# Kernel optimization log

Hardware: AMD Instinct MI355X
Metric: run time of the kernel (lower is better)

Reference implementation:

```python
import jax, jax.numpy as jnp
import numpy as np

B, N, NPOINT, NSAMPLE = 8, 8192, 2048, 64
RADIUS = 0.2
C_IN = 64  # input feature channels; mlp[0]=64 -> 67 after use_xyz concat


def setup_inputs() -> dict:
    key = jax.random.key(0)
    ks = jax.random.split(key, 12)
    xyz = jax.random.uniform(ks[0], (B, N, 3), dtype=jnp.float32)
    features = jax.random.normal(ks[1], (B, N, C_IN), dtype=jnp.float32)
    inds = jax.random.randint(ks[2], (B, NPOINT), 0, N, dtype=jnp.int32)

    def mkw(k, cin, cout):
        return jax.random.normal(k, (cin, cout), jnp.float32) * (1.0 / np.sqrt(cin).astype(np.float32))

    w0 = mkw(ks[3], C_IN + 3, 64)
    w1 = mkw(ks[4], 64, 64)
    w2 = mkw(ks[5], 64, 128)
    # BN (inference) folded into per-channel scale/shift
    s0 = 1.0 + 0.1 * jax.random.normal(ks[6], (64,), jnp.float32)
    t0 = 0.1 * jax.random.normal(ks[7], (64,), jnp.float32)
    s1 = 1.0 + 0.1 * jax.random.normal(ks[8], (64,), jnp.float32)
    t1 = 0.1 * jax.random.normal(ks[9], (64,), jnp.float32)
    s2 = 1.0 + 0.1 * jax.random.normal(ks[10], (128,), jnp.float32)
    t2 = 0.1 * jax.random.normal(ks[11], (128,), jnp.float32)
    return dict(xyz=xyz, features=features, inds=inds,
                w0=w0, s0=s0, t0=t0, w1=w1, s1=s1, t1=t1, w2=w2, s2=s2, t2=t2)


def _ball_query(xyz, new_xyz):
    """First NSAMPLE point indices within RADIUS of each query; pad by repeating
    the first hit (matches CUDA ball_query semantics). xyz:(B,N,3) new_xyz:(B,S,3)."""
    nn = jnp.sum(xyz * xyz, axis=-1)            # (B,N)
    qq = jnp.sum(new_xyz * new_xyz, axis=-1)    # (B,S)
    d2 = qq[:, :, None] + nn[:, None, :] - 2.0 * jnp.einsum('bsc,bnc->bsn', new_xyz, xyz)
    within = d2 < (RADIUS * RADIUS)
    ar = jnp.arange(N, dtype=jnp.int32)
    keyed = jnp.where(within, ar[None, None, :], N)   # out-of-radius -> sentinel N
    keyed = jnp.sort(keyed, axis=-1)[:, :, :NSAMPLE]  # first hits in point order
    idx = jnp.where(keyed == N, keyed[:, :, :1], keyed)
    return jnp.minimum(idx, N - 1)


_gather = jax.vmap(lambda pts, i: pts[i])  # (N,C),(M,) -> (M,C) per batch


def reference(xyz, features, inds, w0, s0, t0, w1, s1, t1, w2, s2, t2):
    new_xyz = _gather(xyz, inds)                              # (B,S,3)
    idx = _ball_query(xyz, new_xyz)                           # (B,S,ns)
    flat = idx.reshape(B, NPOINT * NSAMPLE)
    g_xyz = _gather(xyz, flat).reshape(B, NPOINT, NSAMPLE, 3)
    g_xyz = (g_xyz - new_xyz[:, :, None, :]) / RADIUS         # normalize_xyz
    g_feat = _gather(features, flat).reshape(B, NPOINT, NSAMPLE, C_IN)
    x = jnp.concatenate([g_xyz, g_feat], axis=-1)             # (B,S,ns,C+3)
    for wgt, s, t in ((w0, s0, t0), (w1, s1, t1), (w2, s2, t2)):
        x = jax.nn.relu(jnp.einsum('bpsc,cd->bpsd', x, wgt) * s + t)
    new_features = jnp.max(x, axis=2)                         # max-pool over nsample
    return new_xyz, new_features, inds, idx
```

## Files before the change

kernel.cpp:

```cpp
#include <hip/hip_runtime.h>

#define BB 8
#define NN 8192
#define NPOINT 2048
#define NSAMPLE 64
#define CIN 64
#define RADIUS 0.2f
#define R2 (RADIUS * RADIUS)

#define OFF_NEWXYZ 0
#define OFF_FEAT (BB * NPOINT * 3)
#define OFF_INDS (OFF_FEAT + BB * NPOINT * 128)
#define OFF_IDX (OFF_INDS + BB * NPOINT)

typedef _Float16 half8 __attribute__((ext_vector_type(8)));
typedef _Float16 half4 __attribute__((ext_vector_type(4)));
typedef __fp16 f16x2 __attribute__((ext_vector_type(2)));
typedef float floatx16 __attribute__((ext_vector_type(16)));
typedef unsigned int uint2v __attribute__((ext_vector_type(2)));

#define P0 88
#define P1 72
#define X_LOC 0
#define H_LOC (64 * P0)
#define XH_WAVE (64 * P0 + 64 * P1)
#define WT0_S 0
#define WT1_S (64 * P0)
#define WT2_S (64 * P0 + 64 * P1)

#define QPW_FB 8
#define QPW_G 2

#define WSF16H (BB * NN * CIN)
#define WT0_OFF WSF16H
#define WT1_OFF (WT0_OFF + 64 * 80)
#define WT2_OFF (WT1_OFF + 64 * 64)
#define WS_END (WT2_OFF + 128 * 64)
#define WS_NEED ((size_t)WS_END * 2)

__global__ __launch_bounds__(256) void ballq_kernel(
    const float* __restrict__ xyz, const int* __restrict__ inds,
    float* __restrict__ out, const float* __restrict__ features,
    _Float16* __restrict__ ws16, const float* __restrict__ w0,
    const float* __restrict__ s0, const float* __restrict__ t0,
    const float* __restrict__ w1, const float* __restrict__ s1,
    const float* __restrict__ w2, const float* __restrict__ s2) {
  if (ws16) {
    const int t = blockIdx.x * 256 + threadIdx.x;
    const float4* src = (const float4*)features;
    const float4 a = src[2 * t + 0];
    const float4 b = src[2 * t + 1];
    union {
      half8 v;
      f16x2 p[4];
    } u;
    u.p[0] = __builtin_amdgcn_cvt_pkrtz(a.x, a.y);
    u.p[1] = __builtin_amdgcn_cvt_pkrtz(a.z, a.w);
    u.p[2] = __builtin_amdgcn_cvt_pkrtz(b.x, b.y);
    u.p[3] = __builtin_amdgcn_cvt_pkrtz(b.z, b.w);
    ((half8*)ws16)[t] = u.v;
    if (blockIdx.x == 0) {
      const int tt = threadIdx.x;
      if (tt < 64) {
        const int d = tt;
        const float sd = s0[d], td = t0[d];
        _Float16* row = ws16 + WT0_OFF + d * 80;
        for (int c = 0; c < 80; ++c) {
          float v = 0.0f;
          if (c < 64) v = w0[(3 + c) * 64 + d] * sd;
          else if (c < 67) v = w0[(c - 64) * 64 + d] * sd;
          else if (c == 67) v = td;
          row[c] = (_Float16)v;
        }
      } else if (tt < 128) {
        const int d = tt - 64;
        const float sd = s1[d];
        _Float16* row = ws16 + WT1_OFF + d * 64;
        for (int c = 0; c < 64; ++c) row[c] = (_Float16)(w1[c * 64 + d] * sd);
      } else {
        const int d2 = tt - 128;
        const float sd = s2[d2];
        _Float16* row = ws16 + WT2_OFF + d2 * 64;
        for (int c = 0; c < 64; ++c) row[c] = (_Float16)(w2[c * 128 + d2] * sd);
      }
    }
  }

  __shared__ int sidx[4][2][NSAMPLE];
  const int wave = (blockIdx.x * 256 + threadIdx.x) >> 6;
  const int lane = threadIdx.x & 63;
  const int wid = threadIdx.x >> 6;
  const int q0 = wave * 2, q1 = q0 + 1;
  const int b = q0 >> 11;

  const float* xb = xyz + (size_t)b * NN * 3;
  const int i0 = inds[q0], i1 = inds[q1];
  const float c0x = xb[i0 * 3 + 0], c0y = xb[i0 * 3 + 1], c0z = xb[i0 * 3 + 2];
  const float c1x = xb[i1 * 3 + 0], c1y = xb[i1 * 3 + 1], c1z = xb[i1 * 3 + 2];

  if (lane < 2) {
    const int qq_ = lane ? q1 : q0;
    const int ii = lane ? i1 : i0;
    out[OFF_NEWXYZ + (size_t)qq_ * 3 + 0] = lane ? c1x : c0x;
    out[OFF_NEWXYZ + (size_t)qq_ * 3 + 1] = lane ? c1y : c0y;
    out[OFF_NEWXYZ + (size_t)qq_ * 3 + 2] = lane ? c1z : c0z;
    out[OFF_INDS + qq_] = (float)ii;
  }

  const float qq0 = c0x * c0x + c0y * c0y + c0z * c0z;
  const float qq1 = c1x * c1x + c1y * c1y + c1z * c1z;

  int cnt0 = 0, cnt1 = 0;
  float ax[4], ay[4], az[4];
#pragma unroll
  for (int k = 0; k < 4; ++k) {
    const float* p = xb + (size_t)(k * 64 + lane) * 3;
    ax[k] = p[0];
    ay[k] = p[1];
    az[k] = p[2];
  }
  for (int j0 = 0; j0 < NN; j0 += 256) {
    float bx[4] = {0}, by[4] = {0}, bz[4] = {0};
    const int jn = j0 + 256;
    if (jn < NN) {
#pragma unroll
      for (int k = 0; k < 4; ++k) {
        const float* p = xb + (size_t)(jn + k * 64 + lane) * 3;
        bx[k] = p[0];
        by[k] = p[1];
        bz[k] = p[2];
      }
    }
#pragma unroll
    for (int k = 0; k < 4; ++k) {
      const int j = j0 + k * 64 + lane;
      const float nn_ = ax[k] * ax[k] + ay[k] * ay[k] + az[k] * az[k];
      const float dot0 = c0x * ax[k] + c0y * ay[k] + c0z * az[k];
      const float dot1 = c1x * ax[k] + c1y * ay[k] + c1z * az[k];
      const bool hit0 = (qq0 + nn_ - 2.0f * dot0) < R2;
      const bool hit1 = (qq1 + nn_ - 2.0f * dot1) < R2;
      const unsigned long long m0 = __ballot(hit0);
      const unsigned long long m1 = __ballot(hit1);
      if (hit0) {
        const int pos = cnt0 + (int)__popcll(m0 & ((1ull << lane) - 1ull));
        if (pos < NSAMPLE) sidx[wid][0][pos] = j;
      }
      if (hit1) {
        const int pos = cnt1 + (int)__popcll(m1 & ((1ull << lane) - 1ull));
        if (pos < NSAMPLE) sidx[wid][1][pos] = j;
      }
      cnt0 += (int)__popcll(m0);
      cnt1 += (int)__popcll(m1);
    }
    if (cnt0 >= NSAMPLE && cnt1 >= NSAMPLE) break;
#pragma unroll
    for (int k = 0; k < 4; ++k) {
      ax[k] = bx[k];
      ay[k] = by[k];
      az[k] = bz[k];
    }
  }
  const int v0 = sidx[wid][0][lane < cnt0 ? lane : 0];
  out[OFF_IDX + (size_t)q0 * NSAMPLE + lane] = (float)v0;
  const int v1 = sidx[wid][1][lane < cnt1 ? lane : 0];
  out[OFF_IDX + (size_t)q1 * NSAMPLE + lane] = (float)v1;
}

__device__ inline unsigned int pkru(float a, float b) {
  union {
    f16x2 p;
    unsigned int u;
  } t;
  t.p = __builtin_amdgcn_cvt_pkrtz(fmaxf(a, 0.0f), fmaxf(b, 0.0f));
  return t.u;
}
__device__ inline void build_frags(const floatx16& acc, half8& f0, half8& f1) {
  unsigned int P[4], Q[4];
#pragma unroll
  for (int rg = 0; rg < 4; ++rg) {
    P[rg] = pkru(acc[4 * rg + 0], acc[4 * rg + 1]);
    Q[rg] = pkru(acc[4 * rg + 2], acc[4 * rg + 3]);
  }
  union {
    unsigned int u[4];
    half8 h;
  } o;
  uint2v sp = __builtin_amdgcn_permlane32_swap(P[0], P[1], false, false);
  uint2v sq = __builtin_amdgcn_permlane32_swap(Q[0], Q[1], false, false);
  o.u[0] = sp.x; o.u[1] = sq.x; o.u[2] = sp.y; o.u[3] = sq.y;
  f0 = o.h;
  sp = __builtin_amdgcn_permlane32_swap(P[2], P[3], false, false);
  sq = __builtin_amdgcn_permlane32_swap(Q[2], Q[3], false, false);
  o.u[0] = sp.x; o.u[1] = sq.x; o.u[2] = sp.y; o.u[3] = sq.y;
  f1 = o.h;
}

__global__ __launch_bounds__(64) void mlp_g(
    const float* __restrict__ xyz, const _Float16* __restrict__ ws16,
    const int* __restrict__ inds, const float* __restrict__ t1,
    const float* __restrict__ t2, float* __restrict__ out) {
  __shared__ _Float16 sm[64 * P0];
  const int l = threadIdx.x & 63;
  const int l31 = l & 31;
  const int h5 = l >> 5;
  const int koff = h5 * 8;

  _Float16* xbuf = sm;
  {
    half8 z = {};
    *(half8*)&xbuf[l * P0 + 72] = z;
  }

  const int lb = (blockIdx.x & 7) * ((int)gridDim.x >> 3) + (blockIdx.x >> 3);
  const int wq0 = lb * QPW_G;
  const int b = wq0 >> 11;
  const float* xb = xyz + (size_t)b * NN * 3;
  const _Float16* fb16 = ws16 + (size_t)b * NN * CIN;

  float t2v[4];
#pragma unroll
  for (int ct = 0; ct < 4; ++ct) t2v[ct] = t2[ct * 32 + l31];
  float t1f[2][16];
#pragma unroll
  for (int nt = 0; nt < 2; ++nt)
#pragma unroll
    for (int rg = 0; rg < 4; ++rg) {
      const float4 tq = *(const float4*)(t1 + nt * 32 + 8 * rg + 4 * h5);
      t1f[nt][4 * rg + 0] = tq.x;
      t1f[nt][4 * rg + 1] = tq.y;
      t1f[nt][4 * rg + 2] = tq.z;
      t1f[nt][4 * rg + 3] = tq.w;
    }

  int myidx = (int)out[OFF_IDX + (size_t)wq0 * NSAMPLE + l];
  int indv = inds[wq0];
  float cx = xb[indv * 3 + 0], cy = xb[indv * 3 + 1], cz = xb[indv * 3 + 2];
  float ppx = xb[myidx * 3 + 0], ppy = xb[myidx * 3 + 1],
        ppz = xb[myidx * 3 + 2];

  unsigned long long wbu = (unsigned long long)(ws16 + WT0_OFF);

#pragma unroll 1
  for (int qi = 0; qi < QPW_G; ++qi) {
    const int q = wq0 + qi;
    const int nq = (qi + 1 < QPW_G) ? q + 1 : q;
    asm volatile("" : "+s"(wbu));
    const _Float16* wt0 = (const _Float16*)wbu;
    const _Float16* wt1q = wt0 + 64 * 80;
    const _Float16* wt2q = wt0 + 64 * 80 + 64 * 64;

    half8 gh[8];
#pragma unroll
    for (int i = 0; i < 8; ++i) {
      const int r = (l >> 3) + 8 * i;
      const int sidx = __shfl(myidx, r, 64);
      gh[i] = *(const half8*)(fb16 + (size_t)sidx * CIN + (l & 7) * 8);
    }
    half8 b0w[2][5];
#pragma unroll
    for (int nt = 0; nt < 2; ++nt)
#pragma unroll
      for (int ks = 0; ks < 5; ++ks)
        b0w[nt][ks] =
            *(const half8*)&wt0[(nt * 32 + l31) * 80 + ks * 16 + koff];
    const float fni = out[OFF_IDX + (size_t)nq * NSAMPLE + l];
    const int nindv = inds[nq];

#pragma unroll
    for (int i = 0; i < 8; ++i) {
      const int r = (l >> 3) + 8 * i;
      *(half8*)&xbuf[r * P0 + (l & 7) * 8] = gh[i];
    }
    {
      union {
        half8 v;
        f16x2 p[4];
      } xv;
      xv.p[0] =
          __builtin_amdgcn_cvt_pkrtz((ppx - cx) * 5.0f, (ppy - cy) * 5.0f);
      xv.p[1] = __builtin_amdgcn_cvt_pkrtz((ppz - cz) * 5.0f, 1.0f);
      xv.p[2] = __builtin_amdgcn_cvt_pkrtz(0.0f, 0.0f);
      xv.p[3] = __builtin_amdgcn_cvt_pkrtz(0.0f, 0.0f);
      *(half8*)&xbuf[l * P0 + 64] = xv.v;
    }

    half8 xa1[2][4];
    {
      half8 xa[2][5];
#pragma unroll
      for (int st = 0; st < 2; ++st)
#pragma unroll
        for (int ks = 0; ks < 5; ++ks)
          xa[st][ks] =
              *(const half8*)&xbuf[(st * 32 + l31) * P0 + ks * 16 + koff];
#pragma unroll
      for (int nt = 0; nt < 2; ++nt)
#pragma unroll
        for (int st = 0; st < 2; ++st) {
          floatx16 acc;
#pragma unroll
          for (int i = 0; i < 16; ++i) acc[i] = 0.0f;
#pragma unroll
          for (int ks = 0; ks < 5; ++ks)
            acc = __builtin_amdgcn_mfma_f32_32x32x16_f16(b0w[nt][ks],
                                                         xa[st][ks], acc,
                                                         0, 0, 0);
          build_frags(acc, xa1[st][2 * nt], xa1[st][2 * nt + 1]);
        }
    }

    const int nidxs = (int)fni;
    const float ncx = xb[nindv * 3 + 0];
    const float ncy = xb[nindv * 3 + 1];
    const float ncz = xb[nindv * 3 + 2];
    const float nppx = xb[nidxs * 3 + 0];
    const float nppy = xb[nidxs * 3 + 1];
    const float nppz = xb[nidxs * 3 + 2];

    half8 h1a[2][4];
    {
      half8 b1w[2][4];
#pragma unroll
      for (int nt = 0; nt < 2; ++nt)
#pragma unroll
        for (int ks = 0; ks < 4; ++ks)
          b1w[nt][ks] =
              *(const half8*)&wt1q[(nt * 32 + l31) * 64 + ks * 16 + koff];
#pragma unroll
      for (int nt = 0; nt < 2; ++nt)
#pragma unroll
        for (int st = 0; st < 2; ++st) {
          floatx16 acc;
#pragma unroll
          for (int i = 0; i < 16; ++i) acc[i] = t1f[nt][i];
#pragma unroll
          for (int ks = 0; ks < 4; ++ks)
            acc = __builtin_amdgcn_mfma_f32_32x32x16_f16(b1w[nt][ks],
                                                         xa1[st][ks], acc,
                                                         0, 0, 0);
          build_frags(acc, h1a[st][2 * nt], h1a[st][2 * nt + 1]);
        }
    }

    {
      half8 b2c[4], b2n[4];
#pragma unroll
      for (int ks = 0; ks < 4; ++ks)
        b2c[ks] = *(const half8*)&wt2q[l31 * 64 + ks * 16 + koff];
#pragma unroll
      for (int ct = 0; ct < 4; ++ct) {
        if (ct < 3) {
#pragma unroll
          for (int ks = 0; ks < 4; ++ks)
            b2n[ks] = *(const half8*)&wt2q[((ct + 1) * 32 + l31) * 64 +
                                           ks * 16 + koff];
        }
        floatx16 aA, aB;
#pragma unroll
        for (int i = 0; i < 16; ++i) {
          aA[i] = 0.0f;
          aB[i] = 0.0f;
        }
#pragma unroll
        for (int ks = 0; ks < 4; ++ks) {
          aA = __builtin_amdgcn_mfma_f32_32x32x16_f16(h1a[0][ks], b2c[ks],
                                                      aA, 0, 0, 0);
          aB = __builtin_amdgcn_mfma_f32_32x32x16_f16(h1a[1][ks], b2c[ks],
                                                      aB, 0, 0, 0);
        }
        float m = fmaxf(aA[0], aB[0]);
#pragma unroll
        for (int i = 1; i < 16; ++i) m = fmaxf(m, fmaxf(aA[i], aB[i]));
        float v = fmaxf(m + t2v[ct], 0.0f);
        v = fmaxf(v, __shfl_xor(v, 32, 64));
        if (l < 32) out[OFF_FEAT + (size_t)q * 128 + ct * 32 + l] = v;
#pragma unroll
        for (int ks = 0; ks < 4; ++ks) b2c[ks] = b2n[ks];
      }
    }

    myidx = nidxs;
    cx = ncx; cy = ncy; cz = ncz;
    ppx = nppx; ppy = nppy; ppz = nppz;
  }
}

__global__ __launch_bounds__(128, 2) void mlp_fb(
    const float* __restrict__ xyz, const float* __restrict__ features,
    const int* __restrict__ inds,
    const float* __restrict__ w0, const float* __restrict__ s0,
    const float* __restrict__ t0, const float* __restrict__ w1,
    const float* __restrict__ s1, const float* __restrict__ t1,
    const float* __restrict__ w2, const float* __restrict__ s2,
    const float* __restrict__ t2, float* __restrict__ out) {
  __shared__ _Float16 sm[2 * XH_WAVE];
  const int tid = threadIdx.x;
  const int w = tid >> 6;
  const int l = tid & 63;
  const int l31 = l & 31;
  const int h5 = l >> 5;
  const int koff = h5 * 8;

  {
    const int d = tid >> 1, hf = tid & 1;
    const float sd0 = s0[d], td0 = t0[d], sd1 = s1[d];
#pragma unroll
    for (int j = 0; j < 44; ++j) {
      const int c = hf * 44 + j;
      float v = 0.0f;
      if (c < 64) v = w0[(3 + c) * 64 + d] * sd0;
      else if (c < 67) v = w0[(c - 64) * 64 + d] * sd0;
      else if (c == 67) v = td0;
      sm[WT0_S + d * P0 + c] = (_Float16)v;
    }
#pragma unroll
    for (int j = 0; j < 32; ++j) {
      const int c = hf * 32 + j;
      sm[WT1_S + d * P1 + c] = (_Float16)(w1[c * 64 + d] * sd1);
    }
    const int ch = tid;
    const float sch = s2[ch];
#pragma unroll
    for (int c = 0; c < 64; ++c)
      sm[WT2_S + ch * P1 + c] = (_Float16)(w2[c * 128 + ch] * sch);
  }
  __syncthreads();

  half8 b0f[2][5], b1f[2][4], b2f[4][4];
#pragma unroll
  for (int nt = 0; nt < 2; ++nt)
#pragma unroll
    for (int ks = 0; ks < 5; ++ks)
      b0f[nt][ks] =
          *(const half8*)&sm[WT0_S + (nt * 32 + l31) * P0 + ks * 16 + koff];
#pragma unroll
  for (int nt = 0; nt < 2; ++nt)
#pragma unroll
    for (int ks = 0; ks < 4; ++ks)
      b1f[nt][ks] =
          *(const half8*)&sm[WT1_S + (nt * 32 + l31) * P1 + ks * 16 + koff];
#pragma unroll
  for (int ct = 0; ct < 4; ++ct)
#pragma unroll
    for (int ks = 0; ks < 4; ++ks)
      b2f[ct][ks] =
          *(const half8*)&sm[WT2_S + (ct * 32 + l31) * P1 + ks * 16 + koff];
  const float t1v0 = t1[l31];
  const float t1v1 = t1[32 + l31];
  float t2v[4];
#pragma unroll
  for (int ct = 0; ct < 4; ++ct) t2v[ct] = t2[ct * 32 + l31];
  __syncthreads();

  _Float16* xbuf = sm + w * XH_WAVE + X_LOC;
  _Float16* hbuf = sm + w * XH_WAVE + H_LOC;
  {
    half8 z = {};
    *(half8*)&xbuf[l * P0 + 72] = z;
  }

  const int lb = (blockIdx.x & 7) * ((int)gridDim.x >> 3) + (blockIdx.x >> 3);
  const int wq0 = (lb * 2 + w) * QPW_FB;
  const int b = wq0 >> 11;
  const float* xb = xyz + (size_t)b * NN * 3;
  const float* fbase = features + (size_t)b * NN * CIN;

  int myidx = (int)out[OFF_IDX + (size_t)wq0 * NSAMPLE + l];
  int indv = inds[wq0];
  float cx = xb[indv * 3 + 0], cy = xb[indv * 3 + 1], cz = xb[indv * 3 + 2];
  float ppx = xb[myidx * 3 + 0], ppy = xb[myidx * 3 + 1],
        ppz = xb[myidx * 3 + 2];

#pragma unroll 1
  for (int qi = 0; qi < QPW_FB; ++qi) {
    const int q = wq0 + qi;
    const int nq = (qi + 1 < QPW_FB) ? q + 1 : q;

    float4 g[16];
#pragma unroll
    for (int i = 0; i < 16; ++i) {
      const int s = (l >> 2) + 16 * (i & 3);
      const int c = (l & 3) + 4 * (i >> 2);
      const int sidx = __shfl(myidx, s, 64);
      g[i] = *(const float4*)(fbase + (size_t)sidx * CIN + 4 * c);
    }
    const float fni = out[OFF_IDX + (size_t)nq * NSAMPLE + l];
    const int nindv = inds[nq];

#pragma unroll
    for (int i = 0; i < 16; ++i) {
      const int s = (l >> 2) + 16 * (i & 3);
      const int c = (l & 3) + 4 * (i >> 2);
      union {
        half4 v;
        f16x2 p[2];
      } hv;
      hv.p[0] = __builtin_amdgcn_cvt_pkrtz(g[i].x, g[i].y);
      hv.p[1] = __builtin_amdgcn_cvt_pkrtz(g[i].z, g[i].w);
      *(half4*)&xbuf[s * P0 + 4 * c] = hv.v;
    }
    {
      union {
        half8 v;
        f16x2 p[4];
      } xv;
      xv.p[0] =
          __builtin_amdgcn_cvt_pkrtz((ppx - cx) * 5.0f, (ppy - cy) * 5.0f);
      xv.p[1] = __builtin_amdgcn_cvt_pkrtz((ppz - cz) * 5.0f, 1.0f);
      xv.p[2] = __builtin_amdgcn_cvt_pkrtz(0.0f, 0.0f);
      xv.p[3] = __builtin_amdgcn_cvt_pkrtz(0.0f, 0.0f);
      *(half8*)&xbuf[l * P0 + 64] = xv.v;
    }

    {
      half8 xa[2][5];
#pragma unroll
      for (int st = 0; st < 2; ++st)
#pragma unroll
        for (int ks = 0; ks < 5; ++ks)
          xa[st][ks] =
              *(const half8*)&xbuf[(st * 32 + l31) * P0 + ks * 16 + koff];
#pragma unroll
      for (int nt = 0; nt < 2; ++nt)
#pragma unroll
        for (int st = 0; st < 2; ++st) {
          floatx16 acc;
#pragma unroll
          for (int i = 0; i < 16; ++i) acc[i] = 0.0f;
#pragma unroll
          for (int ks = 0; ks < 5; ++ks)
            acc = __builtin_amdgcn_mfma_f32_32x32x16_f16(xa[st][ks],
                                                         b0f[nt][ks], acc,
                                                         0, 0, 0);
#pragma unroll
          for (int reg = 0; reg < 16; ++reg) {
            const int row = st * 32 + (reg & 3) + 8 * (reg >> 2) + 4 * h5;
            hbuf[row * P1 + nt * 32 + l31] = (_Float16)fmaxf(acc[reg], 0.0f);
          }
        }
    }

    const int nidxs = (int)fni;
    const float ncx = xb[nindv * 3 + 0];
    const float ncy = xb[nindv * 3 + 1];
    const float ncz = xb[nindv * 3 + 2];
    const float nppx = xb[nidxs * 3 + 0];
    const float nppy = xb[nidxs * 3 + 1];
    const float nppz = xb[nidxs * 3 + 2];

    {
      half8 ha[2][4];
#pragma unroll
      for (int st = 0; st < 2; ++st)
#pragma unroll
        for (int ks = 0; ks < 4; ++ks)
          ha[st][ks] =
              *(const half8*)&hbuf[(st * 32 + l31) * P1 + ks * 16 + koff];
#pragma unroll
      for (int nt = 0; nt < 2; ++nt) {
        const float tt = nt ? t1v1 : t1v0;
#pragma unroll
        for (int st = 0; st < 2; ++st) {
          floatx16 acc;
#pragma unroll
          for (int i = 0; i < 16; ++i) acc[i] = 0.0f;
#pragma unroll
          for (int ks = 0; ks < 4; ++ks)
            acc = __builtin_amdgcn_mfma_f32_32x32x16_f16(ha[st][ks],
                                                         b1f[nt][ks], acc,
                                                         0, 0, 0);
#pragma unroll
          for (int reg = 0; reg < 16; ++reg) {
            const int row = st * 32 + (reg & 3) + 8 * (reg >> 2) + 4 * h5;
            xbuf[row * P0 + nt * 32 + l31] =
                (_Float16)fmaxf(acc[reg] + tt, 0.0f);
          }
        }
      }
    }

    {
      half8 h1a[2][4];
#pragma unroll
      for (int st = 0; st < 2; ++st)
#pragma unroll
        for (int ks = 0; ks < 4; ++ks)
          h1a[st][ks] =
              *(const half8*)&xbuf[(st * 32 + l31) * P0 + ks * 16 + koff];
#pragma unroll
      for (int ct = 0; ct < 4; ++ct) {
        floatx16 aA, aB;
#pragma unroll
        for (int i = 0; i < 16; ++i) {
          aA[i] = 0.0f;
          aB[i] = 0.0f;
        }
#pragma unroll
        for (int ks = 0; ks < 4; ++ks) {
          aA = __builtin_amdgcn_mfma_f32_32x32x16_f16(h1a[0][ks], b2f[ct][ks],
                                                      aA, 0, 0, 0);
          aB = __builtin_amdgcn_mfma_f32_32x32x16_f16(h1a[1][ks], b2f[ct][ks],
                                                      aB, 0, 0, 0);
        }
        float m = fmaxf(aA[0], aB[0]);
#pragma unroll
        for (int i = 1; i < 16; ++i) m = fmaxf(m, fmaxf(aA[i], aB[i]));
        float v = fmaxf(m + t2v[ct], 0.0f);
        v = fmaxf(v, __shfl_xor(v, 32, 64));
        if (l < 32) out[OFF_FEAT + (size_t)q * 128 + ct * 32 + l] = v;
      }
    }

    myidx = nidxs;
    cx = ncx; cy = ncy; cz = ncz;
    ppx = nppx; ppy = nppy; ppz = nppz;
  }
}

extern "C" void kernel_launch(void* const* d_in, const int* in_sizes, int n_in,
                              void* d_out, int out_size, void* d_ws,
                              size_t ws_size, hipStream_t stream) {
  const float* xyz = (const float*)d_in[0];
  const float* features = (const float*)d_in[1];
  const int* inds = (const int*)d_in[2];
  const float* w0 = (const float*)d_in[3];
  const float* s0 = (const float*)d_in[4];
  const float* t0 = (const float*)d_in[5];
  const float* w1 = (const float*)d_in[6];
  const float* s1 = (const float*)d_in[7];
  const float* t1 = (const float*)d_in[8];
  const float* w2 = (const float*)d_in[9];
  const float* s2 = (const float*)d_in[10];
  const float* t2 = (const float*)d_in[11];
  float* out = (float*)d_out;

  _Float16* ws16 = (ws_size >= WS_NEED) ? (_Float16*)d_ws : nullptr;

  const int nquery = BB * NPOINT;
  ballq_kernel<<<nquery / 8, 256, 0, stream>>>(xyz, inds, out, features, ws16,
                                               w0, s0, t0, w1, s1, w2, s2);
  if (ws16) {
    mlp_g<<<nquery / QPW_G, 64, 0, stream>>>(xyz, ws16, inds, t1, t2, out);
  } else {
    mlp_fb<<<nquery / (2 * QPW_FB), 128, 0, stream>>>(
        xyz, features, inds, w0, s0, t0, w1, s1, t1, w2, s2, t2, out);
  }
}
```

Baseline: 183.2 us.

## Load gathered features straight into MFMA fragments and fold layer-1 bias into weights

The main MLP kernel now gathers fp16 feature rows directly into register MFMA operand fragments, so it no longer stages them through LDS. The xyz offsets are built via lane shuffles, and the kernel uses no shared memory at all. The layer-1 bias moves into the padded weight tile (column 67) and is applied with an extra MFMA against a constant bias fragment, replacing the per-lane bias registers. The launch bound now requests higher occupancy. The fallback kernel gets the same bias folding. In exchange, the kernel does more strided global loads per lane and one extra MFMA per tile.

```diff
diff --git a/kernel.cpp b/kernel.cpp
--- a/kernel.cpp
+++ b/kernel.cpp
@@ -21,20 +21,19 @@
 
 #define P0 88
 #define P1 72
-#define X_LOC 0
-#define H_LOC (64 * P0)
-#define XH_WAVE (64 * P0 + 64 * P1)
 #define WT0_S 0
 #define WT1_S (64 * P0)
-#define WT2_S (64 * P0 + 64 * P1)
-
-#define QPW_FB 8
-#define QPW_G 2
+#define WT2_S (WT1_S + 64 * P0)
+#define SM_H (WT2_S + 128 * P1)
+#define XSL (64 * P0)
+
+#define QPW 8
+#define QPW_Z 2
 
 #define WSF16H (BB * NN * CIN)
 #define WT0_OFF WSF16H
 #define WT1_OFF (WT0_OFF + 64 * 80)
-#define WT2_OFF (WT1_OFF + 64 * 64)
+#define WT2_OFF (WT1_OFF + 64 * 80)
 #define WS_END (WT2_OFF + 128 * 64)
 #define WS_NEED ((size_t)WS_END * 2)
 
@@ -44,7 +43,8 @@
     _Float16* __restrict__ ws16, const float* __restrict__ w0,
     const float* __restrict__ s0, const float* __restrict__ t0,
     const float* __restrict__ w1, const float* __restrict__ s1,
-    const float* __restrict__ w2, const float* __restrict__ s2) {
+    const float* __restrict__ t1, const float* __restrict__ w2,
+    const float* __restrict__ s2) {
   if (ws16) {
     const int t = blockIdx.x * 256 + threadIdx.x;
     const float4* src = (const float4*)features;
@@ -74,9 +74,14 @@
         }
       } else if (tt < 128) {
         const int d = tt - 64;
-        const float sd = s1[d];
-        _Float16* row = ws16 + WT1_OFF + d * 64;
-        for (int c = 0; c < 64; ++c) row[c] = (_Float16)(w1[c * 64 + d] * sd);
+        const float sd = s1[d], td = t1[d];
+        _Float16* row = ws16 + WT1_OFF + d * 80;
+        for (int c = 0; c < 80; ++c) {
+          float v = 0.0f;
+          if (c < 64) v = w1[c * 64 + d] * sd;
+          else if (c == 67) v = td;
+          row[c] = (_Float16)v;
+        }
       } else {
         const int d2 = tt - 128;
         const float sd = s2[d2];
@@ -195,24 +200,17 @@
   f1 = o.h;
 }
 
-__global__ __launch_bounds__(64) void mlp_g(
+__global__ __launch_bounds__(64, 3) void mlp_z(
     const float* __restrict__ xyz, const _Float16* __restrict__ ws16,
-    const int* __restrict__ inds, const float* __restrict__ t1,
-    const float* __restrict__ t2, float* __restrict__ out) {
-  __shared__ _Float16 sm[64 * P0];
+    const int* __restrict__ inds, const float* __restrict__ t2,
+    float* __restrict__ out) {
   const int l = threadIdx.x & 63;
   const int l31 = l & 31;
   const int h5 = l >> 5;
   const int koff = h5 * 8;
 
-  _Float16* xbuf = sm;
-  {
-    half8 z = {};
-    *(half8*)&xbuf[l * P0 + 72] = z;
-  }
-
   const int lb = (blockIdx.x & 7) * ((int)gridDim.x >> 3) + (blockIdx.x >> 3);
-  const int wq0 = lb * QPW_G;
+  const int wq0 = lb * QPW_Z;
   const int b = wq0 >> 11;
   const float* xb = xyz + (size_t)b * NN * 3;
   const _Float16* fb16 = ws16 + (size_t)b * NN * CIN;
@@ -220,17 +218,8 @@
   float t2v[4];
 #pragma unroll
   for (int ct = 0; ct < 4; ++ct) t2v[ct] = t2[ct * 32 + l31];
-  float t1f[2][16];
-#pragma unroll
-  for (int nt = 0; nt < 2; ++nt)
-#pragma unroll
-    for (int rg = 0; rg < 4; ++rg) {
-      const float4 tq = *(const float4*)(t1 + nt * 32 + 8 * rg + 4 * h5);
-      t1f[nt][4 * rg + 0] = tq.x;
-      t1f[nt][4 * rg + 1] = tq.y;
-      t1f[nt][4 * rg + 2] = tq.z;
-      t1f[nt][4 * rg + 3] = tq.w;
-    }
+  half8 bias_f = {};
+  if (h5 == 0) bias_f[3] = (_Float16)1.0f;
 
   int myidx = (int)out[OFF_IDX + (size_t)wq0 * NSAMPLE + l];
   int indv = inds[wq0];
@@ -241,35 +230,243 @@
   unsigned long long wbu = (unsigned long long)(ws16 + WT0_OFF);
 
 #pragma unroll 1
-  for (int qi = 0; qi < QPW_G; ++qi) {
+  for (int qi = 0; qi < QPW_Z; ++qi) {
     const int q = wq0 + qi;
-    const int nq = (qi + 1 < QPW_G) ? q + 1 : q;
+    const int nq = (qi + 1 < QPW_Z) ? q + 1 : q;
     asm volatile("" : "+s"(wbu));
     const _Float16* wt0 = (const _Float16*)wbu;
     const _Float16* wt1q = wt0 + 64 * 80;
-    const _Float16* wt2q = wt0 + 64 * 80 + 64 * 64;
-
-    half8 gh[8];
-#pragma unroll
-    for (int i = 0; i < 8; ++i) {
-      const int r = (l >> 3) + 8 * i;
-      const int sidx = __shfl(myidx, r, 64);
-      gh[i] = *(const half8*)(fb16 + (size_t)sidx * CIN + (l & 7) * 8);
-    }
-    half8 b0w[2][5];
-#pragma unroll
-    for (int nt = 0; nt < 2; ++nt)
-#pragma unroll
-      for (int ks = 0; ks < 5; ++ks)
-        b0w[nt][ks] =
-            *(const half8*)&wt0[(nt * 32 + l31) * 80 + ks * 16 + koff];
+    const _Float16* wt2q = wt0 + 64 * 80 + 64 * 80;
+
+    half8 xa[2][5];
+#pragma unroll
+    for (int st = 0; st < 2; ++st) {
+      const int sIdx = __shfl(myidx, st * 32 + l31, 64);
+      const _Float16* base = fb16 + (size_t)sIdx * CIN + koff;
+#pragma unroll
+      for (int ks = 0; ks < 4; ++ks) xa[st][ks] = *(const half8*)(base + ks * 16);
+    }
     const float fni = out[OFF_IDX + (size_t)nq * NSAMPLE + l];
     const int nindv = inds[nq];
-
-#pragma unroll
-    for (int i = 0; i < 8; ++i) {
-      const int r = (l >> 3) + 8 * i;
-      *(half8*)&xbuf[r * P0 + (l & 7) * 8] = gh[i];
+#pragma unroll
+    for (int st = 0; st < 2; ++st) {
+      const float sx = __shfl(ppx, st * 32 + l31, 64);
+      const float sy = __shfl(ppy, st * 32 + l31, 64);
+      const float sz = __shfl(ppz, st * 32 + l31, 64);
+      union {
+        half8 v;
+        f16x2 p[4];
+      } xv;
+      xv.p[0] = __builtin_amdgcn_cvt_pkrtz((sx - cx) * 5.0f, (sy - cy) * 5.0f);
+      xv.p[1] = __builtin_amdgcn_cvt_pkrtz((sz - cz) * 5.0f, 1.0f);
+      xv.p[2] = __builtin_amdgcn_cvt_pkrtz(0.0f, 0.0f);
+      xv.p[3] = __builtin_amdgcn_cvt_pkrtz(0.0f, 0.0f);
+      half8 z = {};
+      xa[st][4] = (h5 == 0) ? xv.v : z;
+    }
+
+    half8 xa1[2][4];
+#pragma unroll
+    for (int nt = 0; nt < 2; ++nt) {
+      half8 w0f[5];
+#pragma unroll
+      for (int ks = 0; ks < 5; ++ks)
+        w0f[ks] = *(const half8*)&wt0[(nt * 32 + l31) * 80 + ks * 16 + koff];
+#pragma unroll
+      for (int st = 0; st < 2; ++st) {
+        floatx16 acc;
+#pragma unroll
+        for (int i = 0; i < 16; ++i) acc[i] = 0.0f;
+#pragma unroll
+        for (int ks = 0; ks < 5; ++ks)
+          acc = __builtin_amdgcn_mfma_f32_32x32x16_f16(w0f[ks], xa[st][ks],
+                                                       acc, 0, 0, 0);
+        build_frags(acc, xa1[st][2 * nt], xa1[st][2 * nt + 1]);
+      }
+    }
+
+    const int nidxs = (int)fni;
+    const float ncx = xb[nindv * 3 + 0];
+    const float ncy = xb[nindv * 3 + 1];
+    const float ncz = xb[nindv * 3 + 2];
+    const float nppx = xb[nidxs * 3 + 0];
+    const float nppy = xb[nidxs * 3 + 1];
+    const float nppz = xb[nidxs * 3 + 2];
+
+    half8 h1a[2][4];
+#pragma unroll
+    for (int nt = 0; nt < 2; ++nt) {
+      half8 w1f[5];
+#pragma unroll
+      for (int ks = 0; ks < 5; ++ks)
+        w1f[ks] = *(const half8*)&wt1q[(nt * 32 + l31) * 80 + ks * 16 + koff];
+#pragma unroll
+      for (int st = 0; st < 2; ++st) {
+        floatx16 acc;
+#pragma unroll
+        for (int i = 0; i < 16; ++i) acc[i] = 0.0f;
+#pragma unroll
+        for (int ks = 0; ks < 4; ++ks)
+          acc = __builtin_amdgcn_mfma_f32_32x32x16_f16(w1f[ks], xa1[st][ks],
+                                                       acc, 0, 0, 0);
+        acc = __builtin_amdgcn_mfma_f32_32x32x16_f16(w1f[4], bias_f, acc,
+                                                     0, 0, 0);
+        build_frags(acc, h1a[st][2 * nt], h1a[st][2 * nt + 1]);
+      }
+    }
+
+    {
+      half8 b2c[4], b2n[4];
+#pragma unroll
+      for (int ks = 0; ks < 4; ++ks)
+        b2c[ks] = *(const half8*)&wt2q[l31 * 64 + ks * 16 + koff];
+#pragma unroll
+      for (int ct = 0; ct < 4; ++ct) {
+        if (ct < 3) {
+#pragma unroll
+          for (int ks = 0; ks < 4; ++ks)
+            b2n[ks] = *(const half8*)&wt2q[((ct + 1) * 32 + l31) * 64 +
+                                           ks * 16 + koff];
+        }
+        floatx16 aA, aB;
+#pragma unroll
+        for (int i = 0; i < 16; ++i) {
+          aA[i] = 0.0f;
+          aB[i] = 0.0f;
+        }
+#pragma unroll
+        for (int ks = 0; ks < 4; ++ks) {
+          aA = __builtin_amdgcn_mfma_f32_32x32x16_f16(h1a[0][ks], b2c[ks],
+                                                      aA, 0, 0, 0);
+          aB = __builtin_amdgcn_mfma_f32_32x32x16_f16(h1a[1][ks], b2c[ks],
+                                                      aB, 0, 0, 0);
+        }
+        float m = fmaxf(aA[0], aB[0]);
+#pragma unroll
+        for (int i = 1; i < 16; ++i) m = fmaxf(m, fmaxf(aA[i], aB[i]));
+        float v = fmaxf(m + t2v[ct], 0.0f);
+        v = fmaxf(v, __shfl_xor(v, 32, 64));
+        if (l < 32) out[OFF_FEAT + (size_t)q * 128 + ct * 32 + l] = v;
+#pragma unroll
+        for (int ks = 0; ks < 4; ++ks) b2c[ks] = b2n[ks];
+      }
+    }
+
+    myidx = nidxs;
+    cx = ncx; cy = ncy; cz = ncz;
+    ppx = nppx; ppy = nppy; ppz = nppz;
+  }
+}
+
+__global__ __launch_bounds__(128, 2) void mlp_r(
+    const float* __restrict__ xyz, const float* __restrict__ features,
+    const int* __restrict__ inds,
+    const float* __restrict__ w0, const float* __restrict__ s0,
+    const float* __restrict__ t0, const float* __restrict__ w1,
+    const float* __restrict__ s1, const float* __restrict__ t1,
+    const float* __restrict__ w2, const float* __restrict__ s2,
+    const float* __restrict__ t2, float* __restrict__ out) {
+  __shared__ _Float16 sm[SM_H];
+  const int tid = threadIdx.x;
+  const int w = tid >> 6;
+  const int l = tid & 63;
+  const int l31 = l & 31;
+  const int h5 = l >> 5;
+  const int koff = h5 * 8;
+
+  {
+    const int d = tid >> 1, hf = tid & 1;
+    const float sd0 = s0[d], td0 = t0[d], sd1 = s1[d], td1 = t1[d];
+#pragma unroll
+    for (int j = 0; j < 44; ++j) {
+      const int c = hf * 44 + j;
+      float v = 0.0f;
+      if (c < 64) v = w0[(3 + c) * 64 + d] * sd0;
+      else if (c < 67) v = w0[(c - 64) * 64 + d] * sd0;
+      else if (c == 67) v = td0;
+      sm[WT0_S + d * P0 + c] = (_Float16)v;
+      float v1 = 0.0f;
+      if (c < 64) v1 = w1[c * 64 + d] * sd1;
+      else if (c == 67) v1 = td1;
+      sm[WT1_S + d * P0 + c] = (_Float16)v1;
+    }
+    const int ch = tid;
+    const float sch = s2[ch];
+#pragma unroll
+    for (int c = 0; c < 64; ++c)
+      sm[WT2_S + ch * P1 + c] = (_Float16)(w2[c * 128 + ch] * sch);
+  }
+  __syncthreads();
+
+  half8 b0f[2][5], b1f[2][5], b2f[4][4];
+#pragma unroll
+  for (int nt = 0; nt < 2; ++nt)
+#pragma unroll
+    for (int ks = 0; ks < 5; ++ks) {
+      b0f[nt][ks] =
+          *(const half8*)&sm[WT0_S + (nt * 32 + l31) * P0 + ks * 16 + koff];
+      b1f[nt][ks] =
+          *(const half8*)&sm[WT1_S + (nt * 32 + l31) * P0 + ks * 16 + koff];
+    }
+#pragma unroll
+  for (int ct = 0; ct < 4; ++ct)
+#pragma unroll
+    for (int ks = 0; ks < 4; ++ks)
+      b2f[ct][ks] =
+          *(const half8*)&sm[WT2_S + (ct * 32 + l31) * P1 + ks * 16 + koff];
+  float t2v[4];
+#pragma unroll
+  for (int ct = 0; ct < 4; ++ct) t2v[ct] = t2[ct * 32 + l31];
+  __syncthreads();
+
+  half8 bias_f = {};
+  if (h5 == 0) bias_f[3] = (_Float16)1.0f;
+
+  _Float16* xbuf = sm + w * XSL;
+  {
+    half8 z = {};
+    *(half8*)&xbuf[l * P0 + 72] = z;
+  }
+
+  const int lb = (blockIdx.x & 7) * ((int)gridDim.x >> 3) + (blockIdx.x >> 3);
+  const int wq0 = (lb * 2 + w) * QPW;
+  const int b = wq0 >> 11;
+  const float* xb = xyz + (size_t)b * NN * 3;
+  const float* fbase = features + (size_t)b * NN * CIN;
+
+  int myidx = (int)out[OFF_IDX + (size_t)wq0 * NSAMPLE + l];
+  int indv = inds[wq0];
+  float cx = xb[indv * 3 + 0], cy = xb[indv * 3 + 1], cz = xb[indv * 3 + 2];
+  float ppx = xb[myidx * 3 + 0], ppy = xb[myidx * 3 + 1],
+        ppz = xb[myidx * 3 + 2];
+
+#pragma unroll 1
+  for (int qi = 0; qi < QPW; ++qi) {
+    const int q = wq0 + qi;
+    const int nq = (qi + 1 < QPW) ? q + 1 : q;
+
+    float4 g[16];
+#pragma unroll
+    for (int i = 0; i < 16; ++i) {
+      const int s = (l >> 2) + 16 * (i & 3);
+      const int c = (l & 3) + 4 * (i >> 2);
+      const int sidx = __shfl(myidx, s, 64);
+      g[i] = *(const float4*)(fbase + (size_t)sidx * CIN + 4 * c);
+    }
+    const float fni = out[OFF_IDX + (size_t)nq * NSAMPLE + l];
+    const int nindv = inds[nq];
+
+#pragma unroll
+    for (int i = 0; i < 16; ++i) {
+      const int s = (l >> 2) + 16 * (i & 3);
+      const int c = (l & 3) + 4 * (i >> 2);
+      union {
+        half4 v;
+        f16x2 p[2];
+      } hv;
+      hv.p[0] = __builtin_amdgcn_cvt_pkrtz(g[i].x, g[i].y);
+      hv.p[1] = __builtin_amdgcn_cvt_pkrtz(g[i].z, g[i].w);
+      *(half4*)&xbuf[s * P0 + 4 * c] = hv.v;
     }
     {
       union {
@@ -302,7 +499,7 @@
           for (int i = 0; i < 16; ++i) acc[i] = 0.0f;
 #pragma unroll
           for (int ks = 0; ks < 5; ++ks)
-            acc = __builtin_amdgcn_mfma_f32_32x32x16_f16(b0w[nt][ks],
+            acc = __builtin_amdgcn_mfma_f32_32x32x16_f16(b0f[nt][ks],
                                                          xa[st][ks], acc,
                                                          0, 0, 0);
           build_frags(acc, xa1[st][2 * nt], xa1[st][2 * nt + 1]);
@@ -319,274 +516,25 @@
 
     half8 h1a[2][4];
     {
-      half8 b1w[2][4];
-#pragma unroll
-      for (int nt = 0; nt < 2; ++nt)
-#pragma unroll
-        for (int ks = 0; ks < 4; ++ks)
-          b1w[nt][ks] =
-              *(const half8*)&wt1q[(nt * 32 + l31) * 64 + ks * 16 + koff];
 #pragma unroll
       for (int nt = 0; nt < 2; ++nt)
 #pragma unroll
         for (int st = 0; st < 2; ++st) {
           floatx16 acc;
 #pragma unroll
-          for (int i = 0; i < 16; ++i) acc[i] = t1f[nt][i];
+          for (int i = 0; i < 16; ++i) acc[i] = 0.0f;
 #pragma unroll
           for (int ks = 0; ks < 4; ++ks)
-            acc = __builtin_amdgcn_mfma_f32_32x32x16_f16(b1w[nt][ks],
+            acc = __builtin_amdgcn_mfma_f32_32x32x16_f16(b1f[nt][ks],
                                                          xa1[st][ks], acc,
                                                          0, 0, 0);
+          acc = __builtin_amdgcn_mfma_f32_32x32x16_f16(b1f[nt][4], bias_f,
+                                                       acc, 0, 0, 0);
           build_frags(acc, h1a[st][2 * nt], h1a[st][2 * nt + 1]);
         }
     }
 
     {
-      half8 b2c[4], b2n[4];
-#pragma unroll
-      for (int ks = 0; ks < 4; ++ks)
-        b2c[ks] = *(const half8*)&wt2q[l31 * 64 + ks * 16 + koff];
-#pragma unroll
-      for (int ct = 0; ct < 4; ++ct) {
-        if (ct < 3) {
-#pragma unroll
-          for (int ks = 0; ks < 4; ++ks)
-            b2n[ks] = *(const half8*)&wt2q[((ct + 1) * 32 + l31) * 64 +
-                                           ks * 16 + koff];
-        }
-        floatx16 aA, aB;
-#pragma unroll
-        for (int i = 0; i < 16; ++i) {
-          aA[i] = 0.0f;
-          aB[i] = 0.0f;
-        }
-#pragma unroll
-        for (int ks = 0; ks < 4; ++ks) {
-          aA = __builtin_amdgcn_mfma_f32_32x32x16_f16(h1a[0][ks], b2c[ks],
-                                                      aA, 0, 0, 0);
-          aB = __builtin_amdgcn_mfma_f32_32x32x16_f16(h1a[1][ks], b2c[ks],
-                                                      aB, 0, 0, 0);
-        }
-        float m = fmaxf(aA[0], aB[0]);
-#pragma unroll
-        for (int i = 1; i < 16; ++i) m = fmaxf(m, fmaxf(aA[i], aB[i]));
-        float v = fmaxf(m + t2v[ct], 0.0f);
-        v = fmaxf(v, __shfl_xor(v, 32, 64));
-        if (l < 32) out[OFF_FEAT + (size_t)q * 128 + ct * 32 + l] = v;
-#pragma unroll
-        for (int ks = 0; ks < 4; ++ks) b2c[ks] = b2n[ks];
-      }
-    }
-
-    myidx = nidxs;
-    cx = ncx; cy = ncy; cz = ncz;
-    ppx = nppx; ppy = nppy; ppz = nppz;
-  }
-}
-
-__global__ __launch_bounds__(128, 2) void mlp_fb(
-    const float* __restrict__ xyz, const float* __restrict__ features,
-    const int* __restrict__ inds,
-    const float* __restrict__ w0, const float* __restrict__ s0,
-    const float* __restrict__ t0, const float* __restrict__ w1,
-    const float* __restrict__ s1, const float* __restrict__ t1,
-    const float* __restrict__ w2, const float* __restrict__ s2,
-    const float* __restrict__ t2, float* __restrict__ out) {
-  __shared__ _Float16 sm[2 * XH_WAVE];
-  const int tid = threadIdx.x;
-  const int w = tid >> 6;
-  const int l = tid & 63;
-  const int l31 = l & 31;
-  const int h5 = l >> 5;
-  const int koff = h5 * 8;
-
-  {
-    const int d = tid >> 1, hf = tid & 1;
-    const float sd0 = s0[d], td0 = t0[d], sd1 = s1[d];
-#pragma unroll
-    for (int j = 0; j < 44; ++j) {
-      const int c = hf * 44 + j;
-      float v = 0.0f;
-      if (c < 64) v = w0[(3 + c) * 64 + d] * sd0;
-      else if (c < 67) v = w0[(c - 64) * 64 + d] * sd0;
-      else if (c == 67) v = td0;
-      sm[WT0_S + d * P0 + c] = (_Float16)v;
-    }
-#pragma unroll
-    for (int j = 0; j < 32; ++j) {
-      const int c = hf * 32 + j;
-      sm[WT1_S + d * P1 + c] = (_Float16)(w1[c * 64 + d] * sd1);
-    }
-    const int ch = tid;
-    const float sch = s2[ch];
-#pragma unroll
-    for (int c = 0; c < 64; ++c)
-      sm[WT2_S + ch * P1 + c] = (_Float16)(w2[c * 128 + ch] * sch);
-  }
-  __syncthreads();
-
-  half8 b0f[2][5], b1f[2][4], b2f[4][4];
-#pragma unroll
-  for (int nt = 0; nt < 2; ++nt)
-#pragma unroll
-    for (int ks = 0; ks < 5; ++ks)
-      b0f[nt][ks] =
-          *(const half8*)&sm[WT0_S + (nt * 32 + l31) * P0 + ks * 16 + koff];
-#pragma unroll
-  for (int nt = 0; nt < 2; ++nt)
-#pragma unroll
-    for (int ks = 0; ks < 4; ++ks)
-      b1f[nt][ks] =
-          *(const half8*)&sm[WT1_S + (nt * 32 + l31) * P1 + ks * 16 + koff];
-#pragma unroll
-  for (int ct = 0; ct < 4; ++ct)
-#pragma unroll
-    for (int ks = 0; ks < 4; ++ks)
-      b2f[ct][ks] =
-          *(const half8*)&sm[WT2_S + (ct * 32 + l31) * P1 + ks * 16 + koff];
-  const float t1v0 = t1[l31];
-  const float t1v1 = t1[32 + l31];
-  float t2v[4];
-#pragma unroll
-  for (int ct = 0; ct < 4; ++ct) t2v[ct] = t2[ct * 32 + l31];
-  __syncthreads();
-
-  _Float16* xbuf = sm + w * XH_WAVE + X_LOC;
-  _Float16* hbuf = sm + w * XH_WAVE + H_LOC;
-  {
-    half8 z = {};
-    *(half8*)&xbuf[l * P0 + 72] = z;
-  }
-
-  const int lb = (blockIdx.x & 7) * ((int)gridDim.x >> 3) + (blockIdx.x >> 3);
-  const int wq0 = (lb * 2 + w) * QPW_FB;
-  const int b = wq0 >> 11;
-  const float* xb = xyz + (size_t)b * NN * 3;
-  const float* fbase = features + (size_t)b * NN * CIN;
-
-  int myidx = (int)out[OFF_IDX + (size_t)wq0 * NSAMPLE + l];
-  int indv = inds[wq0];
-  float cx = xb[indv * 3 + 0], cy = xb[indv * 3 + 1], cz = xb[indv * 3 + 2];
-  float ppx = xb[myidx * 3 + 0], ppy = xb[myidx * 3 + 1],
-        ppz = xb[myidx * 3 + 2];
-
-#pragma unroll 1
-  for (int qi = 0; qi < QPW_FB; ++qi) {
-    const int q = wq0 + qi;
-    const int nq = (qi + 1 < QPW_FB) ? q + 1 : q;
-
-    float4 g[16];
-#pragma unroll
-    for (int i = 0; i < 16; ++i) {
-      const int s = (l >> 2) + 16 * (i & 3);
-      const int c = (l & 3) + 4 * (i >> 2);
-      const int sidx = __shfl(myidx, s, 64);
-      g[i] = *(const float4*)(fbase + (size_t)sidx * CIN + 4 * c);
-    }
-    const float fni = out[OFF_IDX + (size_t)nq * NSAMPLE + l];
-    const int nindv = inds[nq];
-
-#pragma unroll
-    for (int i = 0; i < 16; ++i) {
-      const int s = (l >> 2) + 16 * (i & 3);
-      const int c = (l & 3) + 4 * (i >> 2);
-      union {
-        half4 v;
-        f16x2 p[2];
-      } hv;
-      hv.p[0] = __builtin_amdgcn_cvt_pkrtz(g[i].x, g[i].y);
-      hv.p[1] = __builtin_amdgcn_cvt_pkrtz(g[i].z, g[i].w);
-      *(half4*)&xbuf[s * P0 + 4 * c] = hv.v;
-    }
-    {
-      union {
-        half8 v;
-        f16x2 p[4];
-      } xv;
-      xv.p[0] =
-          __builtin_amdgcn_cvt_pkrtz((ppx - cx) * 5.0f, (ppy - cy) * 5.0f);
-      xv.p[1] = __builtin_amdgcn_cvt_pkrtz((ppz - cz) * 5.0f, 1.0f);
-      xv.p[2] = __builtin_amdgcn_cvt_pkrtz(0.0f, 0.0f);
-      xv.p[3] = __builtin_amdgcn_cvt_pkrtz(0.0f, 0.0f);
-      *(half8*)&xbuf[l * P0 + 64] = xv.v;
-    }
-
-    {
-      half8 xa[2][5];
-#pragma unroll
-      for (int st = 0; st < 2; ++st)
-#pragma unroll
-        for (int ks = 0; ks < 5; ++ks)
-          xa[st][ks] =
-              *(const half8*)&xbuf[(st * 32 + l31) * P0 + ks * 16 + koff];
-#pragma unroll
-      for (int nt = 0; nt < 2; ++nt)
-#pragma unroll
-        for (int st = 0; st < 2; ++st) {
-          floatx16 acc;
-#pragma unroll
-          for (int i = 0; i < 16; ++i) acc[i] = 0.0f;
-#pragma unroll
-          for (int ks = 0; ks < 5; ++ks)
-            acc = __builtin_amdgcn_mfma_f32_32x32x16_f16(xa[st][ks],
-                                                         b0f[nt][ks], acc,
-                                                         0, 0, 0);
-#pragma unroll
-          for (int reg = 0; reg < 16; ++reg) {
-            const int row = st * 32 + (reg & 3) + 8 * (reg >> 2) + 4 * h5;
-            hbuf[row * P1 + nt * 32 + l31] = (_Float16)fmaxf(acc[reg], 0.0f);
-          }
-        }
-    }
-
-    const int nidxs = (int)fni;
-    const float ncx = xb[nindv * 3 + 0];
-    const float ncy = xb[nindv * 3 + 1];
-    const float ncz = xb[nindv * 3 + 2];
-    const float nppx = xb[nidxs * 3 + 0];
-    const float nppy = xb[nidxs * 3 + 1];
-    const float nppz = xb[nidxs * 3 + 2];
-
-    {
-      half8 ha[2][4];
-#pragma unroll
-      for (int st = 0; st < 2; ++st)
-#pragma unroll
-        for (int ks = 0; ks < 4; ++ks)
-          ha[st][ks] =
-              *(const half8*)&hbuf[(st * 32 + l31) * P1 + ks * 16 + koff];
-#pragma unroll
-      for (int nt = 0; nt < 2; ++nt) {
-        const float tt = nt ? t1v1 : t1v0;
-#pragma unroll
-        for (int st = 0; st < 2; ++st) {
-          floatx16 acc;
-#pragma unroll
-          for (int i = 0; i < 16; ++i) acc[i] = 0.0f;
-#pragma unroll
-          for (int ks = 0; ks < 4; ++ks)
-            acc = __builtin_amdgcn_mfma_f32_32x32x16_f16(ha[st][ks],
-                                                         b1f[nt][ks], acc,
-                                                         0, 0, 0);
-#pragma unroll
-          for (int reg = 0; reg < 16; ++reg) {
-            const int row = st * 32 + (reg & 3) + 8 * (reg >> 2) + 4 * h5;
-            xbuf[row * P0 + nt * 32 + l31] =
-                (_Float16)fmaxf(acc[reg] + tt, 0.0f);
-          }
-        }
-      }
-    }
-
-    {
-      half8 h1a[2][4];
-#pragma unroll
-      for (int st = 0; st < 2; ++st)
-#pragma unroll
-        for (int ks = 0; ks < 4; ++ks)
-          h1a[st][ks] =
-              *(const half8*)&xbuf[(st * 32 + l31) * P0 + ks * 16 + koff];
 #pragma unroll
       for (int ct = 0; ct < 4; ++ct) {
         floatx16 aA, aB;
@@ -638,11 +586,11 @@
 
   const int nquery = BB * NPOINT;
   ballq_kernel<<<nquery / 8, 256, 0, stream>>>(xyz, inds, out, features, ws16,
-                                               w0, s0, t0, w1, s1, w2, s2);
+                                               w0, s0, t0, w1, s1, t1, w2, s2);
   if (ws16) {
-    mlp_g<<<nquery / QPW_G, 64, 0, stream>>>(xyz, ws16, inds, t1, t2, out);
+    mlp_z<<<nquery / QPW_Z, 64, 0, stream>>>(xyz, ws16, inds, t2, out);
   } else {
-    mlp_fb<<<nquery / (2 * QPW_FB), 128, 0, stream>>>(
+    mlp_r<<<nquery / (2 * QPW), 128, 0, stream>>>(
         xyz, features, inds, w0, s0, t0, w1, s1, t1, w2, s2, t2, out);
   }
 }
```

Result: no change. 181.9 us (-0.7%).
